# Kernel tuning notes

Hardware: AMD Instinct MI355X
Metric: run time of the kernel (lower is better)

## Reference

```python
import jax, jax.numpy as jnp
import numpy as np

N = 20000      # nodes
E = 1280000    # edges
F = 42         # num_features (forced equal to mpnn out_channels by the code)
H = 20         # lstm hidden per direction


def setup_inputs() -> dict:
    key = jax.random.key(0)
    ks = jax.random.split(key, 17)
    def rn(k, shape, sc=0.1):
        return jax.random.normal(k, shape, dtype=jnp.float32) * sc
    return {
        "x": rn(ks[0], (N, F), 1.0),
        "edge_index": jax.random.randint(ks[1], (2, E), 0, N),
        "edge_attr": jax.random.uniform(ks[2], (E, 1), dtype=jnp.float32),
        "lin_w": rn(ks[3], (F, 2 * F)),
        "lin_b": rn(ks[4], (F,)),
        "gru_w_ih": rn(ks[5], (3 * F, F)),
        "gru_w_hh": rn(ks[6], (3 * F, F)),
        "gru_b_ih": rn(ks[7], (3 * F,)),
        "gru_b_hh": rn(ks[8], (3 * F,)),
        "lstm_w_ih_f": rn(ks[9], (4 * H, F)),
        "lstm_w_hh_f": rn(ks[10], (4 * H, H)),
        "lstm_b_f": rn(ks[11], (4 * H,)),
        "lstm_w_ih_b": rn(ks[12], (4 * H, F)),
        "lstm_w_hh_b": rn(ks[13], (4 * H, H)),
        "lstm_b_b": rn(ks[14], (4 * H,)),
        "cls_w": rn(ks[15], (1, 2 * H)),
        "cls_b": rn(ks[16], (1,)),
    }


def _lstm_dir(xs, w_ih, w_hh, b):
    # xs: [N, F] treated as a length-N sequence with batch 1
    x_proj = xs @ w_ih.T + b  # [N, 4H] precompute input contribution
    def cell(carry, xp):
        h, c = carry
        g = xp + w_hh @ h                      # [4H]
        i, f, gg, o = jnp.split(g, 4)
        c = jax.nn.sigmoid(f) * c + jax.nn.sigmoid(i) * jnp.tanh(gg)
        h = jax.nn.sigmoid(o) * jnp.tanh(c)
        return (h, c), h
    h0 = jnp.zeros((H,), xs.dtype)
    _, hs = jax.lax.scan(cell, (h0, h0), x_proj)
    return hs  # [N, H]


def reference(x, edge_index, edge_attr, lin_w, lin_b,
              gru_w_ih, gru_w_hh, gru_b_ih, gru_b_hh,
              lstm_w_ih_f, lstm_w_hh_f, lstm_b_f,
              lstm_w_ih_b, lstm_w_hh_b, lstm_b_b,
              cls_w, cls_b):
    n = x.shape[0]
    src, dst = edge_index[0], edge_index[1]
    # --- message: gather x_i (target) / x_j (source), concat-linear, sigmoid gate
    x_i = x[dst]                               # [E, F]
    x_j = x[src]                               # [E, F]
    msg = jnp.concatenate([x_i, x_j], axis=1) @ lin_w.T + lin_b  # [E, F]
    msg = msg * jax.nn.sigmoid(-edge_attr)     # gate on -time_diff, broadcast [E,1]
    # --- aggregate: scatter-add at target nodes
    agg = jax.ops.segment_sum(msg, dst, num_segments=n)  # [N, F]
    # --- GRU, seq_len=1, batch=N, input = hidden init = agg
    gi = agg @ gru_w_ih.T + gru_b_ih           # [N, 3F]
    gh = agg @ gru_w_hh.T + gru_b_hh           # [N, 3F]
    i_r, i_z, i_n = jnp.split(gi, 3, axis=1)
    h_r, h_z, h_n = jnp.split(gh, 3, axis=1)
    r = jax.nn.sigmoid(i_r + h_r)
    z = jax.nn.sigmoid(i_z + h_z)
    ng = jnp.tanh(i_n + r * h_n)
    hx = (1.0 - z) * ng + z * agg              # [N, F]
    # --- bidirectional LSTM over nodes as a sequence (batch=1)
    h_fwd = _lstm_dir(hx, lstm_w_ih_f, lstm_w_hh_f, lstm_b_f)                # [N, H]
    h_bwd = _lstm_dir(hx[::-1], lstm_w_ih_b, lstm_w_hh_b, lstm_b_b)[::-1]    # [N, H]
    h_cat = jnp.concatenate([h_fwd, h_bwd], axis=1)  # [N, 2H]
    return h_cat @ cls_w.T + cls_b             # [N, 1]
```

## Files before the change

kernel.cpp:

```cpp
#include <hip/hip_runtime.h>

#define NN 20000
#define EE 1280000
#define FF 42
#define HH 20
#define PSTR 44

#define CHUNK 50
#define WARM 50
#define NCH 400
#define TT 16

#define NBIN 625
#define BINW 32
#define CAP  2560
#define NCHKB 160
#define CHKE 8000
#define NSC (NBIN*NCHKB)
#define NSB1 ((NSC+255)/256)

__device__ __forceinline__ float fexp2(float x){ return __builtin_amdgcn_exp2f(x); }
__device__ __forceinline__ float frcp(float x){ return __builtin_amdgcn_rcpf(x); }
__device__ __forceinline__ float fsigmoid(float x){ return frcp(1.f + fexp2(-1.442695041f*x)); }
__device__ __forceinline__ float ftanh(float x){ return 2.f*frcp(1.f + fexp2(-2.885390082f*x)) - 1.f; }

__global__ __launch_bounds__(256) void k_nodeproj(
    const float* __restrict__ x, const float* __restrict__ lw,
    float* __restrict__ PA, float* __restrict__ PB)
{
  __shared__ float2 w1S[FF*21];
  __shared__ float2 w2S[FF*21];
  for (int idx=threadIdx.x; idx<FF*21; idx+=256){
    int k = idx/21, fp = idx - 21*k;
    w1S[idx] = make_float2(lw[(2*fp)*84 + k],      lw[(2*fp+1)*84 + k]);
    w2S[idx] = make_float2(lw[(2*fp)*84 + 42 + k], lw[(2*fp+1)*84 + 42 + k]);
  }
  __syncthreads();
  int tid = blockIdx.x*256 + threadIdx.x;
  if (tid >= NN*21) return;
  int n = tid / 21;
  int fp = tid - n*21;
  const float* xr = x + n*FF;
  float2 pa = make_float2(0.f,0.f), pb = make_float2(0.f,0.f);
#pragma unroll 6
  for (int k=0;k<FF;k++){
    float xv = xr[k];
    float2 w1 = w1S[k*21+fp], w2 = w2S[k*21+fp];
    pa.x += w1.x*xv; pa.y += w1.y*xv;
    pb.x += w2.x*xv; pb.y += w2.y*xv;
  }
  ((float2*)(PA + n*PSTR))[fp] = pa;
  ((float2*)(PB + n*PSTR))[fp] = pb;
  if (fp == 0){
    PA[n*PSTR+42] = 0.f; PA[n*PSTR+43] = 0.f;
    PB[n*PSTR+42] = 0.f; PB[n*PSTR+43] = 0.f;
  }
}

__global__ __launch_bounds__(256) void k_binA(const int* __restrict__ dst, int* __restrict__ cnt)
{
  __shared__ unsigned int h[NBIN];
  int blk = blockIdx.x, tid = threadIdx.x;
  for (int i=tid; i<NBIN; i+=256) h[i] = 0;
  __syncthreads();
  const int* d = dst + blk*CHKE;
  for (int i=tid; i<CHKE; i+=256) atomicAdd(&h[d[i]>>5], 1u);
  __syncthreads();
  for (int i=tid; i<NBIN; i+=256) cnt[i*NCHKB + blk] = (int)h[i];
}

__global__ __launch_bounds__(256) void k_scan1(int* __restrict__ cnt, int* __restrict__ bsum)
{
  int b = blockIdx.x, t = threadIdx.x;
  int i = b*256 + t;
  int v = (i < NSC) ? cnt[i] : 0;
  int lane = t & 63, w = t >> 6;
  int x = v;
#pragma unroll
  for (int off=1; off<64; off<<=1){
    int y = __shfl_up(x, off);
    if (lane >= off) x += y;
  }
  __shared__ int wsum[4];
  if (lane == 63) wsum[w] = x;
  __syncthreads();
  int base = 0;
  for (int ww=0; ww<w; ww++) base += wsum[ww];
  int incl = x + base;
  if (i < NSC) cnt[i] = incl - v;
  if (t == 255) bsum[b] = incl;
}

__global__ __launch_bounds__(1024) void k_scan2(const int* __restrict__ bsum, int* __restrict__ boff)
{
  int t = threadIdx.x;
  int v = (t < NSB1) ? bsum[t] : 0;
  int lane = t & 63, w = t >> 6;
  int x = v;
#pragma unroll
  for (int off=1; off<64; off<<=1){
    int y = __shfl_up(x, off);
    if (lane >= off) x += y;
  }
  __shared__ int ws2[16];
  if (lane == 63) ws2[w] = x;
  __syncthreads();
  int base = 0;
  for (int ww=0; ww<w; ww++) base += ws2[ww];
  int incl = x + base;
  if (t < NSB1) boff[t] = incl - v;
}

__global__ __launch_bounds__(256) void k_binC(
    const int* __restrict__ src, const int* __restrict__ dst,
    const float* __restrict__ ea, const int* __restrict__ cnt,
    const int* __restrict__ boff, int2* __restrict__ binned)
{
  __shared__ unsigned int cur[NBIN];
  int blk = blockIdx.x, tid = threadIdx.x;
  for (int i=tid; i<NBIN; i+=256){
    int idx = i*NCHKB + blk;
    cur[i] = (unsigned)(cnt[idx] + boff[idx>>8]);
  }
  __syncthreads();
  for (int i=tid; i<CHKE; i+=256){
    int e = blk*CHKE + i;
    int d = dst[e];
    int s = src[e];
    float g = fsigmoid(-ea[e]);
    unsigned p = atomicAdd(&cur[d>>5], 1u);
    int2 r; r.x = s | ((d & 31) << 16); r.y = __float_as_int(g);
    binned[p] = r;
  }
}

__global__ __launch_bounds__(512, 8) void k_agg(
    const float* __restrict__ PA, const float* __restrict__ PB,
    const int* __restrict__ cnt, const int* __restrict__ boff,
    const int2* __restrict__ binned, const float* __restrict__ lin_b,
    float* __restrict__ agg)
{
  __shared__ int2 edS[CAP];
  __shared__ unsigned int cntL[BINW];
  __shared__ unsigned int offsN[BINW+1];
  __shared__ float lbS[PSTR];

  int b = blockIdx.x, tid = threadIdx.x;
  if (tid < PSTR) lbS[tid] = (tid < FF) ? lin_b[tid] : 0.f;
  int i0g = b*NCHKB;
  int e0 = cnt[i0g] + boff[i0g>>8];
  int e1;
  if (b == NBIN-1) e1 = EE;
  else { int i1g = (b+1)*NCHKB; e1 = cnt[i1g] + boff[i1g>>8]; }
  int cl = e1 - e0; if (cl > CAP) cl = CAP;

  int2 E[5];
  if (tid < BINW) cntL[tid] = 0;
  __syncthreads();
#pragma unroll
  for (int u=0; u<5; u++){
    int i = tid + u*512;
    if (i < cl){
      E[u] = binned[e0+i];
      atomicAdd(&cntL[E[u].x >> 16], 1u);
    }
  }
  __syncthreads();
  if (tid < 64){
    unsigned v = (tid < BINW) ? cntL[tid] : 0u;
    unsigned x = v;
#pragma unroll
    for (int off=1; off<32; off<<=1){
      unsigned y = __shfl_up(x, off);
      if ((tid & 63) >= off) x += y;
    }
    if (tid < BINW) offsN[tid+1] = x;
    if (tid == 0) offsN[0] = 0;
  }
  __syncthreads();
  if (tid < BINW) cntL[tid] = offsN[tid];
  __syncthreads();
#pragma unroll
  for (int u=0; u<5; u++){
    int i = tid + u*512;
    if (i < cl){
      unsigned p = atomicAdd(&cntL[E[u].x >> 16], 1u);
      edS[p] = E[u];
    }
  }
  __syncthreads();

  int w = tid >> 6, lane = tid & 63;
  int grp = lane / 11;
  int fp  = lane - grp*11;
  bool lact = grp < 5;
  unsigned a0[4], aE[4];
  int M = 0;
#pragma unroll
  for (int j=0;j<4;j++){
    int n = w + 8*j;
    a0[j] = offsN[n]; aE[j] = offsN[n+1];
    int len = (int)(aE[j]-a0[j]); if (len > M) M = len;
  }
  float4 acc[4]; float gs[4];
#pragma unroll
  for (int j=0;j<4;j++){ acc[j]=make_float4(0.f,0.f,0.f,0.f); gs[j]=0.f; }
  for (int t=0; t<M; t+=5){
    float4 pv[4]; float gv[4];
#pragma unroll
    for (int j=0;j<4;j++){
      unsigned k = a0[j] + (unsigned)(t + grp);
      bool v = lact && (k < aE[j]);
      unsigned ks = v ? k : 0u;
      int2 Ee = edS[ks];
      gv[j] = v ? __int_as_float(Ee.y) : 0.f;
      pv[j] = ((const float4*)(PB + (Ee.x & 0xFFFF)*PSTR))[fp];
    }
#pragma unroll
    for (int j=0;j<4;j++){
      acc[j].x += gv[j]*pv[j].x;  acc[j].y += gv[j]*pv[j].y;
      acc[j].z += gv[j]*pv[j].z;  acc[j].w += gv[j]*pv[j].w;
      gs[j]    += gv[j];
    }
  }
#pragma unroll
  for (int j=0;j<4;j++){
    float vx=acc[j].x, vy=acc[j].y, vz=acc[j].z, vw=acc[j].w, g=gs[j];
#pragma unroll
    for (int s=1;s<5;s++){
      vx += __shfl(acc[j].x, lane + 11*s);
      vy += __shfl(acc[j].y, lane + 11*s);
      vz += __shfl(acc[j].z, lane + 11*s);
      vw += __shfl(acc[j].w, lane + 11*s);
      g  += __shfl(gs[j],    lane + 11*s);
    }
    if (lane < 11){
      int n = w + 8*j;
      const float4 pa = ((const float4*)(PA + (b*BINW+n)*PSTR))[fp];
      float4 lb = ((const float4*)lbS)[fp];
      float4 o;
      o.x = (pa.x + lb.x)*g + vx;
      o.y = (pa.y + lb.y)*g + vy;
      o.z = (pa.z + lb.z)*g + vz;
      o.w = (pa.w + lb.w)*g + vw;
      ((float4*)(agg + (b*BINW+n)*PSTR))[fp] = o;
    }
  }
}

#define GNOD 64
#define GSTR 45
__global__ __launch_bounds__(1024, 4) void k_gru(
    const float* __restrict__ agg,
    const float* __restrict__ gwih, const float* __restrict__ gwhh,
    const float* __restrict__ gbih, const float* __restrict__ gbhh,
    const float* __restrict__ lwihf, const float* __restrict__ lbf,
    const float* __restrict__ lwihb, const float* __restrict__ lbb,
    float* __restrict__ xpf, float* __restrict__ xpb)
{
  __shared__ float aggL[GNOD*GSTR];
  __shared__ float hxL [GNOD*GSTR];
  int b = blockIdx.x, tid = threadIdx.x;
  int node = tid & 63;
  int n = b*GNOD + node;
  int slot = __builtin_amdgcn_readfirstlane(tid >> 6);

  for (int idx=tid; idx<GNOD*11; idx+=1024){
    int nd = idx/11, c = idx - 11*nd;
    int gn = b*GNOD + nd;
    if (gn < NN){
      float4 v = ((const float4*)(agg + gn*PSTR))[c];
      float* d = aggL + nd*GSTR + 4*c;
      d[0]=v.x; d[1]=v.y; d[2]=v.z; d[3]=v.w;
    }
  }
  __syncthreads();

  bool act = n < NN;
  const float* Arow = aggL + node*GSTR;

#pragma unroll 1
  for (int jj=0; jj<3; jj++){
    int j = slot + 16*jj;
    if (j < FF){
      float ir = gbih[j], iz = gbih[FF+j], inn = gbih[2*FF+j];
      float hr = gbhh[j], hz = gbhh[FF+j], hn  = gbhh[2*FF+j];
      const float* Wi0 = gwih + j*FF;
      const float* Wi1 = gwih + (FF+j)*FF;
      const float* Wi2 = gwih + (2*FF+j)*FF;
      const float* Wh0 = gwhh + j*FF;
      const float* Wh1 = gwhh + (FF+j)*FF;
      const float* Wh2 = gwhh + (2*FF+j)*FF;
#pragma unroll
      for (int k=0;k<FF;k++){
        float a = Arow[k];
        ir += Wi0[k]*a;  iz += Wi1[k]*a;  inn += Wi2[k]*a;
        hr += Wh0[k]*a;  hz += Wh1[k]*a;  hn  += Wh2[k]*a;
      }
      float r  = fsigmoid(ir+hr);
      float z  = fsigmoid(iz+hz);
      float ng = ftanh(inn + r*hn);
      hxL[node*GSTR + j] = (1.f - z)*ng + z*Arow[j];
    }
  }
  __syncthreads();

  const float* Hrow = hxL + node*GSTR;

#pragma unroll 1
  for (int ro=0; ro<10; ro++){
    int gq = slot + 16*ro;
    bool fw = gq < 80;
    int g = fw ? gq : gq - 80;
    const float* Wp = (fw ? lwihf : lwihb) + g*FF;
    float d = fw ? lbf[g] : lbb[g];
#pragma unroll
    for (int k=0;k<FF;k++) d += Wp[k]*Hrow[k];
    if (act){
      float* dstp = fw ? xpf : xpb;
      dstp[n*80 + g] = d;
    }
  }
}

__global__ __launch_bounds__(64) void k_lstm(
    const float* __restrict__ xpf, const float* __restrict__ xpb,
    const float* __restrict__ whhf, const float* __restrict__ whhb,
    float* __restrict__ hf, float* __restrict__ hb)
{
  __shared__ float buf[2][TT*80];
  int b = blockIdx.x;
  int dir = b / NCH;
  int chunk = b - dir*NCH;
  const float* xp  = dir ? xpb  : xpf;
  const float* whh = dir ? whhb : whhf;
  float* hout      = dir ? hb   : hf;

  int lane = threadIdx.x;
  int m = (lane < HH) ? lane : HH-1;
  bool active = lane < HH;

  float Wi[HH], Wf[HH], Wg[HH], Wo[HH];
#pragma unroll
  for (int k=0;k<HH;k++){
    Wi[k] = whh[(     m)*HH + k];
    Wf[k] = whh[(  HH+m)*HH + k];
    Wg[k] = whh[(2*HH+m)*HH + k];
    Wo[k] = whh[(3*HH+m)*HH + k];
  }

  int p0 = chunk*CHUNK;
  int ps = (p0 >= WARM) ? (p0-WARM) : 0;
  int p1 = p0 + CHUNK;
  int steps = p1 - ps;
  int ntiles = (steps + TT - 1)/TT;

  float4 R0,R1,R2,R3,R4;

  auto fetch = [&](int j){
    int a = ps + j*TT;
    long g0;
    if (!dir) g0 = (long)a*80;
    else { int t_lo = NN - a - TT; if (t_lo < 0) t_lo = 0; g0 = (long)t_lo*80; }
    const float* s = xp + g0 + lane*4;
    R0 = *(const float4*)(s);
    R1 = *(const float4*)(s + 256);
    R2 = *(const float4*)(s + 512);
    R3 = *(const float4*)(s + 768);
    R4 = *(const float4*)(s + 1024);
  };
  auto stash = [&](int dbuf){
    float* d = buf[dbuf] + lane*4;
    *(float4*)(d)        = R0;
    *(float4*)(d + 256)  = R1;
    *(float4*)(d + 512)  = R2;
    *(float4*)(d + 768)  = R3;
    *(float4*)(d + 1024) = R4;
  };

  fetch(0); stash(0);
  if (ntiles > 1) fetch(1);

  float c = 0.f;
  float Hs[HH];
#pragma unroll
  for (int k=0;k<HH;k++) Hs[k] = 0.f;

  for (int j=0; j<ntiles; ++j){
    const float* B = buf[j&1];
    int a = ps + j*TT;
    int t_lo = 0;
    if (dir){ t_lo = NN - a - TT; if (t_lo < 0) t_lo = 0; }
#pragma unroll 4
    for (int r=0; r<TT; ++r){
      int p = a + r;
      int row = dir ? (NN-1-p - t_lo) : r;
      const float* Br = B + row*80 + m;
      float xi = Br[0];
      float xf = Br[HH];
      float xg = Br[2*HH];
      float xo = Br[3*HH];
      float ai0=xi, ai1=0.f, af0=xf, af1=0.f, ag0=xg, ag1=0.f, ao0=xo, ao1=0.f;
#pragma unroll
      for (int k=0;k<HH/2;k++){
        ai0 += Wi[2*k]*Hs[2*k];  ai1 += Wi[2*k+1]*Hs[2*k+1];
        af0 += Wf[2*k]*Hs[2*k];  af1 += Wf[2*k+1]*Hs[2*k+1];
        ag0 += Wg[2*k]*Hs[2*k];  ag1 += Wg[2*k+1]*Hs[2*k+1];
        ao0 += Wo[2*k]*Hs[2*k];  ao1 += Wo[2*k+1]*Hs[2*k+1];
      }
      float si = fsigmoid(ai0+ai1);
      float sf = fsigmoid(af0+af1);
      float tg = ftanh(ag0+ag1);
      float so = fsigmoid(ao0+ao1);
      c = sf*c + si*tg;
      float h = so*ftanh(c);
#pragma unroll
      for (int k=0;k<HH;k++)
        Hs[k] = __int_as_float(__builtin_amdgcn_readlane(__float_as_int(h), k));
      if (p >= p0 && p < p1 && active){
        int t = dir ? (NN-1-p) : p;
        hout[t*HH + lane] = h;
      }
    }
    if (j+1 < ntiles){
      stash((j+1)&1);
      if (j+2 < ntiles) fetch(j+2);
    }
  }
}

__global__ __launch_bounds__(256) void k_cls(
    const float* __restrict__ hf, const float* __restrict__ hb,
    const float* __restrict__ cw, const float* __restrict__ cb,
    float* __restrict__ out)
{
  int n = blockIdx.x*256 + threadIdx.x;
  if (n >= NN) return;
  float s = cb[0];
  const float* hfr = hf + n*HH;
  const float* hbr = hb + n*HH;
#pragma unroll
  for (int k=0;k<HH;k++){
    s += hfr[k]*cw[k] + hbr[k]*cw[HH+k];
  }
  out[n] = s;
}

extern "C" void kernel_launch(void* const* d_in, const int* in_sizes, int n_in,
                              void* d_out, int out_size, void* d_ws, size_t ws_size,
                              hipStream_t stream) {
  (void)in_sizes; (void)n_in; (void)out_size; (void)ws_size;
  const float* x      = (const float*)d_in[0];
  const int*   ei     = (const int*)  d_in[1];
  const float* ea     = (const float*)d_in[2];
  const float* lin_w  = (const float*)d_in[3];
  const float* lin_b  = (const float*)d_in[4];
  const float* gwih   = (const float*)d_in[5];
  const float* gwhh   = (const float*)d_in[6];
  const float* gbih   = (const float*)d_in[7];
  const float* gbhh   = (const float*)d_in[8];
  const float* lwihf  = (const float*)d_in[9];
  const float* lwhhf  = (const float*)d_in[10];
  const float* lbf    = (const float*)d_in[11];
  const float* lwihb  = (const float*)d_in[12];
  const float* lwhhb  = (const float*)d_in[13];
  const float* lbb    = (const float*)d_in[14];
  const float* cw     = (const float*)d_in[15];
  const float* cb     = (const float*)d_in[16];
  float* out = (float*)d_out;

  const int* src = ei;
  const int* dst = ei + EE;

  float* PA     = (float*)d_ws;
  float* PB     = PA + NN*PSTR;
  float* agg    = PB + NN*PSTR;
  float* xpf    = agg + NN*PSTR;
  float* xpb    = xpf + NN*80;
  float* hf     = xpb + NN*80;
  float* hb     = hf + NN*HH;
  int2*  binned = (int2*)(hb + NN*HH);
  int*   cnt    = (int*)(binned + EE);
  int*   bsum   = cnt + NSC;
  int*   boff   = bsum + NSB1;

  k_nodeproj<<<(NN*21 + 255)/256, 256, 0, stream>>>(x, lin_w, PA, PB);
  k_binA<<<NCHKB, 256, 0, stream>>>(dst, cnt);
  k_scan1<<<NSB1, 256, 0, stream>>>(cnt, bsum);
  k_scan2<<<1, 1024, 0, stream>>>(bsum, boff);
  k_binC<<<NCHKB, 256, 0, stream>>>(src, dst, ea, cnt, boff, binned);
  k_agg<<<NBIN, 512, 0, stream>>>(PA, PB, cnt, boff, binned, lin_b, agg);
  k_gru<<<(NN + GNOD - 1)/GNOD, 1024, 0, stream>>>(agg, gwih, gwhh, gbih, gbhh,
                                                   lwihf, lbf, lwihb, lbb, xpf, xpb);
  k_lstm<<<2*NCH, 64, 0, stream>>>(xpf, xpb, lwhhf, lwhhb, hf, hb);
  k_cls<<<(NN + 255)/256, 256, 0, stream>>>(hf, hb, cw, cb, out);
}
```

Measured before the change: 264.8 us.

## Split LSTM gate rows across wave halves and halve sequence chunk size

The LSTM recurrence kernel now spreads the four gate rows over both 32-lane halves of the wavefront. Each lane computes two gate dot products instead of four, and the partner gate values are exchanged with a lane shuffle. Chunk size is halved, which doubles the number of blocks. Input projections are prefetched one step ahead, and the next tile is stashed at the start of each tile rather than the end. In exchange, the fixed 50-step warm-up now costs a larger share of each chunk, and each step adds cross-lane shuffle latency.

```diff
diff --git a/kernel.cpp b/kernel.cpp
--- a/kernel.cpp
+++ b/kernel.cpp
@@ -6,9 +6,9 @@
 #define HH 20
 #define PSTR 44
 
-#define CHUNK 50
+#define CHUNK 25
 #define WARM 50
-#define NCH 400
+#define NCH 800
 #define TT 16
 
 #define NBIN 625
@@ -337,17 +337,22 @@
   float* hout      = dir ? hb   : hf;
 
   int lane = threadIdx.x;
-  int m = (lane < HH) ? lane : HH-1;
-  bool active = lane < HH;
-
-  float Wi[HH], Wf[HH], Wg[HH], Wo[HH];
-#pragma unroll
-  for (int k=0;k<HH;k++){
-    Wi[k] = whh[(     m)*HH + k];
-    Wf[k] = whh[(  HH+m)*HH + k];
-    Wg[k] = whh[(2*HH+m)*HH + k];
-    Wo[k] = whh[(3*HH+m)*HH + k];
-  }
+  int m = lane & 31;
+  int half = lane >> 5;
+  int mm = (m < HH) ? m : HH-1;
+  int rowA = half*40 + mm;
+  int rowB = rowA + HH;
+  float2 WA[10], WB[10];
+#pragma unroll
+  for (int kk=0;kk<10;kk++){
+    WA[kk] = make_float2(whh[rowA*HH+2*kk], whh[rowA*HH+2*kk+1]);
+    WB[kk] = make_float2(whh[rowB*HH+2*kk], whh[rowB*HH+2*kk+1]);
+  }
+  const float cE = half ? -2.885390082f : -1.442695041f;
+  const float cM = half ? 2.f : 1.f;
+  const float cA = half ? -1.f : 0.f;
+  int colA = rowA;
+  int colB = rowB;
 
   int p0 = chunk*CHUNK;
   int ps = (p0 >= WARM) ? (p0-WARM) : 0;
@@ -356,7 +361,6 @@
   int ntiles = (steps + TT - 1)/TT;
 
   float4 R0,R1,R2,R3,R4;
-
   auto fetch = [&](int j){
     int a = ps + j*TT;
     long g0;
@@ -381,50 +385,64 @@
   fetch(0); stash(0);
   if (ntiles > 1) fetch(1);
 
-  float c = 0.f;
-  float Hs[HH];
-#pragma unroll
-  for (int k=0;k<HH;k++) Hs[k] = 0.f;
+  float c = 0.f, h = 0.f;
+  float2 H[10];
+#pragma unroll
+  for (int kk=0;kk<10;kk++) H[kk] = make_float2(0.f, 0.f);
+
+  int t_lo0 = 0;
+  if (dir){ t_lo0 = NN - ps - TT; if (t_lo0 < 0) t_lo0 = 0; }
+  int row0 = dir ? (NN-1-ps - t_lo0) : 0;
+  float nxA = buf[0][row0*80 + colA];
+  float nxB = buf[0][row0*80 + colB];
 
   for (int j=0; j<ntiles; ++j){
-    const float* B = buf[j&1];
+    if (j+1 < ntiles) stash((j+1)&1);
+    if (j+2 < ntiles) fetch(j+2);
+    const float* B  = buf[j&1];
+    const float* Bn = buf[(j+1)&1];
     int a = ps + j*TT;
     int t_lo = 0;
     if (dir){ t_lo = NN - a - TT; if (t_lo < 0) t_lo = 0; }
+    int aN = a + TT;
+    int t_loN = 0;
+    if (dir){ t_loN = NN - aN - TT; if (t_loN < 0) t_loN = 0; }
 #pragma unroll 4
     for (int r=0; r<TT; ++r){
       int p = a + r;
-      int row = dir ? (NN-1-p - t_lo) : r;
-      const float* Br = B + row*80 + m;
-      float xi = Br[0];
-      float xf = Br[HH];
-      float xg = Br[2*HH];
-      float xo = Br[3*HH];
-      float ai0=xi, ai1=0.f, af0=xf, af1=0.f, ag0=xg, ag1=0.f, ao0=xo, ao1=0.f;
-#pragma unroll
-      for (int k=0;k<HH/2;k++){
-        ai0 += Wi[2*k]*Hs[2*k];  ai1 += Wi[2*k+1]*Hs[2*k+1];
-        af0 += Wf[2*k]*Hs[2*k];  af1 += Wf[2*k+1]*Hs[2*k+1];
-        ag0 += Wg[2*k]*Hs[2*k];  ag1 += Wg[2*k+1]*Hs[2*k+1];
-        ao0 += Wo[2*k]*Hs[2*k];  ao1 += Wo[2*k+1]*Hs[2*k+1];
+      float xA = nxA, xB = nxB;
+      if (r+1 < TT){
+        int rowN = dir ? (NN-1-(p+1) - t_lo) : (r+1);
+        nxA = B[rowN*80 + colA];
+        nxB = B[rowN*80 + colB];
+      } else if (j+1 < ntiles){
+        int rowN = dir ? (NN-1-aN - t_loN) : 0;
+        nxA = Bn[rowN*80 + colA];
+        nxB = Bn[rowN*80 + colB];
       }
-      float si = fsigmoid(ai0+ai1);
-      float sf = fsigmoid(af0+af1);
-      float tg = ftanh(ag0+ag1);
-      float so = fsigmoid(ao0+ao1);
-      c = sf*c + si*tg;
-      float h = so*ftanh(c);
-#pragma unroll
-      for (int k=0;k<HH;k++)
-        Hs[k] = __int_as_float(__builtin_amdgcn_readlane(__float_as_int(h), k));
-      if (p >= p0 && p < p1 && active){
+      float aA0=xA, aA1=0.f, aB0=xB, aB1=0.f;
+#pragma unroll
+      for (int kk=0;kk<10;kk++){
+        aA0 += WA[kk].x*H[kk].x;  aA1 += WA[kk].y*H[kk].y;
+        aB0 += WB[kk].x*H[kk].x;  aB1 += WB[kk].y*H[kk].y;
+      }
+      float gA = aA0+aA1, gB = aB0+aB1;
+      float actA = cM*frcp(1.f + fexp2(cE*gA)) + cA;
+      float actB = frcp(1.f + fexp2(-1.442695041f*gB));
+      float gT = __shfl_xor(actA, 32);
+      float oT = __shfl_xor(actB, 32);
+      c = actB*c + actA*gT;
+      h = oT*ftanh(c);
+#pragma unroll
+      for (int kk=0;kk<10;kk++){
+        float va = __int_as_float(__builtin_amdgcn_readlane(__float_as_int(h), 2*kk));
+        float vb = __int_as_float(__builtin_amdgcn_readlane(__float_as_int(h), 2*kk+1));
+        H[kk] = make_float2(va, vb);
+      }
+      if (p >= p0 && p < p1 && lane < HH){
         int t = dir ? (NN-1-p) : p;
         hout[t*HH + lane] = h;
       }
-    }
-    if (j+1 < ntiles){
-      stash((j+1)&1);
-      if (j+2 < ntiles) fetch(j+2);
     }
   }
 }
```

Result: faster. 248.1 us (-6.3%).
